# Performance work log

Hardware: AMD Instinct MI355X
Metric: run time of the kernel (lower is better)

## Reference

```python
import jax, jax.numpy as jnp
import numpy as np

X = 512; Y = 512; C = 3; NK = 15
DT = 0.2; DD = 2; SIGMA = 0.95
THETA_X = 2.0; N_EXP = 2.0
K_SIZE = 16

# mesh-grid positions, cell centers at +0.5 (matches construct_mesh_grid)
POS = (jnp.stack(jnp.meshgrid(jnp.arange(X), jnp.arange(Y), indexing='ij'), axis=-1) + 0.5).astype(jnp.float32)  # [X,Y,2]


def _dwconv(img, k):
    # img [X,Y,C'] -> depthwise 3x3 cross-correlation with 'same' zero padding (matches torch conv2d)
    z = img.transpose(2, 0, 1)[None]                      # [1,C',X,Y]
    kern = jnp.tile(k[None, None], (z.shape[1], 1, 1, 1))  # [C',1,3,3]
    out = jax.lax.conv_general_dilated(z, kern, (1, 1), 'SAME', feature_group_count=z.shape[1])
    return out[0].transpose(1, 2, 0)


def _sobel(img):
    # returns [X,Y,2,C'] with (sy, sx) stacked on axis 2, matching torch code order
    kx = jnp.array([[-1., 0., 1.], [-2., 0., 2.], [-1., 0., 1.]], jnp.float32)
    return jnp.stack([_dwconv(img, kx.T), _dwconv(img, kx)], axis=2)


def _reintegrate(grid, F):
    # Flow-Lenia reintegration tracking: 25 static roll offsets, fused accumulation
    ma = DD - SIGMA
    mu = POS[..., None] + jnp.clip(DT * F, -ma, ma)  # [X,Y,2,C]
    mu = jnp.clip(mu, SIGMA, X - SIGMA)
    clip_hi = min(1.0, 2.0 * SIGMA)
    inv_area = 1.0 / (4.0 * SIGMA ** 2)
    acc = jnp.zeros_like(grid)
    for dx in range(-DD, DD + 1):
        for dy in range(-DD, DD + 1):
            gridR = jnp.roll(grid, (dx, dy), (0, 1))
            muR = jnp.roll(mu, (dx, dy), (0, 1))
            sz = 0.5 - jnp.abs(POS[..., None] - muR) + SIGMA
            area = jnp.prod(jnp.clip(sz, 0.0, clip_hi), axis=2) * inv_area  # [X,Y,C]
            acc = acc + gridR * area
    return acc


def _forward(x, Ks, m, s, h, w_c1, c0):
    # spectral kernels: normalize, fftshift, fft2 (matches construct_kernels)
    Ksn = Ks / Ks.sum(axis=(0, 1), keepdims=True)
    fk = jnp.fft.fft2(jnp.fft.fftshift(Ksn, axes=(0, 1)), axes=(0, 1))  # [X,Y,NK] complex
    fXs = jnp.fft.fft2(x, axes=(0, 1))
    Us = jnp.fft.ifft2(fk * fXs[:, :, c0], axes=(0, 1)).real            # [X,Y,NK]
    # growth * h (note: h appears again inside w_c1, faithful to original double multiply)
    Gs = (jnp.exp(-(((Us - m) / s) ** 2) * 0.5) * 2.0 - 1.0) * h
    Hs = jnp.einsum('xyk,kc->xyc', Gs, w_c1)                             # [X,Y,C]
    grad_u = _sobel(Hs)                                                  # [X,Y,2,C]
    grad_x = _sobel(x.sum(-1, keepdims=True))                            # [X,Y,2,1]
    alpha = jnp.clip((x[:, :, None, :] / THETA_X) ** N_EXP, 0.0, 1.0)    # [X,Y,1,C]
    F = grad_u * (1.0 - alpha) - grad_x * alpha                          # [X,Y,2,C]
    return _reintegrate(x, F)


def setup_inputs() -> dict:
    key = jax.random.key(0)
    k1, k2, k3, k4, k5 = jax.random.split(key, 5)
    x = jax.random.uniform(k1, (X, Y, C), jnp.float32)
    # ring kernels per construct_kernels (non-sparse branch)
    mg = np.mgrid[-X // 2:X // 2, -Y // 2:Y // 2]
    base = np.linalg.norm(mg, axis=0).astype(np.float32)
    ks_list = []
    for i in range(NK):
        r = 0.6 + 0.04 * i
        D = base / ((K_SIZE + 15) * r)
        sig = 0.5 * (np.tanh(-(D - 1.0) * 10.0 / 2.0) + 1.0)
        bell = np.exp(-(D - 0.5) ** 2 / 0.15)
        ks_list.append(sig * bell)
    Ks = jnp.asarray(np.stack(ks_list, -1).astype(np.float32))
    m = 0.1 + 0.3 * jax.random.uniform(k2, (NK,), jnp.float32)
    s = 0.03 + 0.15 * jax.random.uniform(k3, (NK,), jnp.float32)
    h = 0.3 + 0.7 * jax.random.uniform(k4, (NK,), jnp.float32)
    c0 = jax.random.randint(k5, (NK,), 0, C, jnp.int32)
    c1 = jnp.arange(NK) % C
    w_c1 = jax.nn.one_hot(c1, C, dtype=jnp.float32) * h[:, None]
    return {"x": x, "Ks": Ks, "m": m, "s": s, "h": h, "w_c1": w_c1, "c0": c0}


def reference(x, Ks, m, s, h, w_c1, c0):
    return _forward(x, Ks, m, s, h, w_c1, c0)
```

## Files before the change

kernel.cpp:

```cpp
#include <hip/hip_runtime.h>
#include <math.h>

#define NPIX 262144
#define NKER 15
#define PI_F 3.14159265358979323846f
#define HW 264
#define CS 578
#define SK(n) ((n) + ((n) >> 3))

__device__ __forceinline__ float2 cadd(float2 a, float2 b) { return make_float2(a.x + b.x, a.y + b.y); }
__device__ __forceinline__ float2 csub(float2 a, float2 b) { return make_float2(a.x - b.x, a.y - b.y); }
__device__ __forceinline__ float2 cmul(float2 a, float2 b) {
  return make_float2(a.x * b.x - a.y * b.y, a.x * b.y + a.y * b.x);
}

__device__ __forceinline__ void fft_roots(int lane, float2* w1, float2* wh) {
  float s, c;
  sincosf(-2.0f * PI_F * (float)lane / 512.0f, &s, &c);
  *w1 = make_float2(c, s);
  int h = lane & ~7;
  *wh = make_float2(__shfl(c, h, 64), __shfl(s, h, 64));
}

template <bool INV>
__device__ __forceinline__ void dft8(float2 a[8]) {
  const float R = 0.70710678118654752f;
  float2 t0 = cadd(a[0], a[4]), u0 = csub(a[0], a[4]);
  float2 t1 = cadd(a[1], a[5]), u1 = csub(a[1], a[5]);
  float2 t2 = cadd(a[2], a[6]), u2 = csub(a[2], a[6]);
  float2 t3 = cadd(a[3], a[7]), u3 = csub(a[3], a[7]);
  u1 = INV ? make_float2(R * (u1.x - u1.y), R * (u1.x + u1.y))
           : make_float2(R * (u1.x + u1.y), R * (u1.y - u1.x));
  u2 = INV ? make_float2(-u2.y, u2.x) : make_float2(u2.y, -u2.x);
  u3 = INV ? make_float2(-R * (u3.x + u3.y), R * (u3.x - u3.y))
           : make_float2(R * (u3.y - u3.x), -R * (u3.x + u3.y));
  float2 e0 = cadd(t0, t2), f0 = csub(t0, t2);
  float2 e1 = cadd(t1, t3), f1 = csub(t1, t3);
  f1 = INV ? make_float2(-f1.y, f1.x) : make_float2(f1.y, -f1.x);
  float2 g0 = cadd(u0, u2), h0 = csub(u0, u2);
  float2 g1 = cadd(u1, u3), h1 = csub(u1, u3);
  h1 = INV ? make_float2(-h1.y, h1.x) : make_float2(h1.y, -h1.x);
  a[0] = cadd(e0, e1); a[4] = csub(e0, e1);
  a[2] = cadd(f0, f1); a[6] = csub(f0, f1);
  a[1] = cadd(g0, g1); a[5] = csub(g0, g1);
  a[3] = cadd(h0, h1); a[7] = csub(h0, h1);
}

template <bool INV>
__device__ __forceinline__ void fft512_r8(float2 a[8], float2* buf, int lane,
                                          float2 w1, float2 wh) {
  float2 wa = INV ? make_float2(w1.x, -w1.y) : w1;
  float2 wb = INV ? make_float2(wh.x, -wh.y) : wh;
  dft8<INV>(a);
  {
    float2 tq = wa;
    a[1] = cmul(a[1], tq);
#pragma unroll
    for (int q = 2; q < 8; ++q) { tq = cmul(tq, wa); a[q] = cmul(a[q], tq); }
  }
#pragma unroll
  for (int q = 0; q < 8; ++q) buf[9 * lane + q] = a[q];
#pragma unroll
  for (int q = 0; q < 8; ++q) a[q] = buf[SK(lane + 64 * q)];
  dft8<INV>(a);
  {
    float2 tq = wb;
    a[1] = cmul(a[1], tq);
#pragma unroll
    for (int q = 2; q < 8; ++q) { tq = cmul(tq, wb); a[q] = cmul(a[q], tq); }
  }
  int h = lane & ~7;
  int b2 = 9 * h + (lane - h);
#pragma unroll
  for (int q = 0; q < 8; ++q) buf[b2 + 9 * q] = a[q];
#pragma unroll
  for (int q = 0; q < 8; ++q) a[q] = buf[SK(lane + 64 * q)];
  dft8<INV>(a);
}

__device__ __forceinline__ void split_store_halfplane(float2 a[8], float2* buf, int lane,
                                                      float2* d0, float2* d1) {
#pragma unroll
  for (int q = 0; q < 8; ++q) buf[SK(lane + 64 * q)] = a[q];
#pragma unroll
  for (int q = 0; q < 4; ++q) {
    int v = lane + 64 * q;
    int mir = (512 - v) & 511;
    float2 P = a[q];
    float2 Qc = buf[SK(mir)];
    float2 Q = make_float2(Qc.x, -Qc.y);
    d0[v] = make_float2(0.5f * (P.x + Q.x), 0.5f * (P.y + Q.y));
    d1[v] = make_float2(0.5f * (P.y - Q.y), -0.5f * (P.x - Q.x));
  }
  if (lane == 0) {
    float2 P = a[4];
    d0[256] = make_float2(P.x, 0.f);
    d1[256] = make_float2(P.y, 0.f);
  }
}

__global__ void rows_all(const float* __restrict__ Ks, const float* __restrict__ x,
                         float* __restrict__ partial, float2* __restrict__ AkH,
                         float2* __restrict__ AxH) {
  __shared__ float krow[512 * NKER];
  __shared__ float2 scr[8][CS];
  __shared__ float psum[480];
  int t = threadIdx.x, wave = t >> 6, lane = t & 63;
  float2 w1, wh;
  fft_roots(lane, &w1, &wh);
  if (blockIdx.x < 512) {
    int b = blockIdx.x;
    int rs = (b + 256) & 511;
    const float2* src = (const float2*)Ks + (size_t)rs * 3840;
    float2* kr2 = (float2*)krow;
    for (int i = t; i < 3840; i += 512) kr2[i] = src[i];
    __syncthreads();
    if (t < 480) {
      int k = t >> 5, yg = t & 31;
      float s = 0.f;
      int base = yg * 16;
#pragma unroll
      for (int y = 0; y < 16; ++y) s += krow[(base + y) * NKER + k];
      psum[t] = s;
    }
    {
      int k1 = 2 * wave, k2 = k1 + 1;
      float2 a[8];
#pragma unroll
      for (int q = 0; q < 8; ++q) {
        int ys = (lane + 64 * q + 256) & 511;
        float re = krow[ys * NKER + k1];
        float im = (k2 < NKER) ? krow[ys * NKER + k2] : 0.f;
        a[q] = make_float2(re, im);
      }
      fft512_r8<false>(a, &scr[wave][0], lane, w1, wh);
      float2* d0 = AkH + ((size_t)k1 * 512 + b) * HW;
      float2* d1 = AkH + ((size_t)k2 * 512 + b) * HW;
      split_store_halfplane(a, &scr[wave][0], lane, d0, d1);
    }
    __syncthreads();
    if (t < NKER) {
      float s = 0.f;
#pragma unroll
      for (int g = 0; g < 32; ++g) s += psum[(t << 5) + g];
      partial[b * 16 + t] = s;
    }
  } else {
    int job = (blockIdx.x - 512) * 8 + wave;
    int c = job >> 8;
    int rp = job & 255;
    int r0 = rp, r1 = rp + 256;
    float2 a[8];
#pragma unroll
    for (int q = 0; q < 8; ++q) {
      int y = lane + 64 * q;
      a[q] = make_float2(x[((size_t)r0 * 512 + y) * 3 + c],
                         x[((size_t)r1 * 512 + y) * 3 + c]);
    }
    fft512_r8<false>(a, &scr[wave][0], lane, w1, wh);
    float2* d0 = AxH + ((size_t)c * 512 + r0) * HW;
    float2* d1 = AxH + ((size_t)c * 512 + r1) * HW;
    split_store_halfplane(a, &scr[wave][0], lane, d0, d1);
  }
}

__global__ void fused_cols(float2* __restrict__ AkH, const float2* __restrict__ AxH,
                           const int* __restrict__ c0, const float* __restrict__ partial,
                           float* __restrict__ sums) {
  __shared__ float2 buf[8 * CS];
  __shared__ float red[512];
  int t = threadIdx.x;
  if (blockIdx.x == 33) {
    if (blockIdx.y != 0) return;
    int k = t & 15, g = t >> 4;
    float acc = 0.f;
    for (int b = g; b < 512; b += 32) acc += partial[b * 16 + k];
    red[t] = acc;
    __syncthreads();
    if (t < 16) {
      float s = 0.f;
#pragma unroll
      for (int g2 = 0; g2 < 32; ++g2) s += red[g2 * 16 + t];
      sums[t] = s;
    }
    return;
  }
  int col0 = blockIdx.x * 8, k = blockIdx.y;
  int c = t >> 6, lane = t & 63;
  float2 w1, wh;
  fft_roots(lane, &w1, &wh);
  const float2* bx = AxH + (size_t)c0[k] * 512 * HW;
  float2* bk = AkH + (size_t)k * 512 * HW;
#pragma unroll
  for (int u = 0; u < 8; ++u) {
    int idx = (u << 9) + t;
    int row = idx >> 3, cc = idx & 7;
    buf[cc * CS + SK(row)] = bx[(size_t)row * HW + col0 + cc];
  }
  __syncthreads();
  float2 xh[8];
#pragma unroll
  for (int q = 0; q < 8; ++q) xh[q] = buf[c * CS + SK(lane + 64 * q)];
  fft512_r8<false>(xh, &buf[c * CS], lane, w1, wh);
  __syncthreads();
#pragma unroll
  for (int u = 0; u < 8; ++u) {
    int idx = (u << 9) + t;
    int row = idx >> 3, cc = idx & 7;
    buf[cc * CS + SK(row)] = bk[(size_t)row * HW + col0 + cc];
  }
  __syncthreads();
  float2 a[8];
#pragma unroll
  for (int q = 0; q < 8; ++q) a[q] = buf[c * CS + SK(lane + 64 * q)];
  fft512_r8<false>(a, &buf[c * CS], lane, w1, wh);
#pragma unroll
  for (int q = 0; q < 8; ++q) a[q] = cmul(a[q], xh[q]);
  fft512_r8<true>(a, &buf[c * CS], lane, w1, wh);
#pragma unroll
  for (int q = 0; q < 8; ++q) buf[c * CS + SK(lane + 64 * q)] = a[q];
  __syncthreads();
#pragma unroll
  for (int u = 0; u < 8; ++u) {
    int idx = (u << 9) + t;
    int row = idx >> 3, cc = idx & 7;
    bk[(size_t)row * HW + col0 + cc] = buf[cc * CS + SK(row)];
  }
}

__global__ void irows_growth_combine(const float2* __restrict__ AkH,
                                     const float* __restrict__ sums,
                                     const float* __restrict__ m, const float* __restrict__ s,
                                     const float* __restrict__ h, const float* __restrict__ w,
                                     float* __restrict__ Hs) {
  __shared__ float2 scr[8][CS];
  __shared__ float accL[4][3][512];
  __shared__ float mk[16], isk[16], hk[16], wk[16][3], sck[16];
  int t = threadIdx.x, wave = t >> 6, lane = t & 63;
  int row = blockIdx.x;
  if (t < NKER) {
    mk[t] = m[t]; isk[t] = 1.0f / s[t]; hk[t] = h[t];
    sck[t] = 1.0f / (sums[t] * 262144.0f);
    wk[t][0] = w[t * 3 + 0]; wk[t][1] = w[t * 3 + 1]; wk[t][2] = w[t * 3 + 2];
  }
  __syncthreads();
  float2 w1, wh;
  fft_roots(lane, &w1, &wh);
  float acc[3][8];
#pragma unroll
  for (int cc = 0; cc < 3; ++cc)
#pragma unroll
    for (int q = 0; q < 8; ++q) acc[cc][q] = 0.f;
  {
    int slot = wave;
    int k1 = 2 * slot, k2 = 2 * slot + 1;
    bool dual = (k2 < NKER);
    const float2* p1 = AkH + ((size_t)k1 * 512 + row) * HW;
    const float2* p2 = AkH + ((size_t)(dual ? k2 : k1) * 512 + row) * HW;
    float2 a[8];
#pragma unroll
    for (int q = 0; q < 8; ++q) {
      int v = lane + 64 * q;
      if (v <= 256) {
        float2 A1 = p1[v];
        float2 A2 = dual ? p2[v] : make_float2(0.f, 0.f);
        a[q] = make_float2(A1.x - A2.y, A1.y + A2.x);
      } else {
        int mi = 512 - v;
        float2 A1 = p1[mi];
        float2 A2 = dual ? p2[mi] : make_float2(0.f, 0.f);
        a[q] = make_float2(A1.x + A2.y, -A1.y + A2.x);
      }
    }
    fft512_r8<true>(a, &scr[wave][0], lane, w1, wh);
    float m1 = mk[k1], i1 = isk[k1], h1 = hk[k1], s1 = sck[k1];
    float w10 = wk[k1][0], w11 = wk[k1][1], w12 = wk[k1][2];
#pragma unroll
    for (int q = 0; q < 8; ++q) {
      float tt = (a[q].x * s1 - m1) * i1;
      float g = (expf(-0.5f * tt * tt) * 2.0f - 1.0f) * h1;
      acc[0][q] += g * w10; acc[1][q] += g * w11; acc[2][q] += g * w12;
    }
    if (dual) {
      float m2 = mk[k2], i2 = isk[k2], h2 = hk[k2], s2 = sck[k2];
      float w20 = wk[k2][0], w21 = wk[k2][1], w22 = wk[k2][2];
#pragma unroll
      for (int q = 0; q < 8; ++q) {
        float tt = (a[q].y * s2 - m2) * i2;
        float g = (expf(-0.5f * tt * tt) * 2.0f - 1.0f) * h2;
        acc[0][q] += g * w20; acc[1][q] += g * w21; acc[2][q] += g * w22;
      }
    }
  }
  if (wave < 4) {
#pragma unroll
    for (int cc = 0; cc < 3; ++cc)
#pragma unroll
      for (int q = 0; q < 8; ++q) accL[wave][cc][lane + 64 * q] = acc[cc][q];
  }
  __syncthreads();
  if (wave >= 4) {
#pragma unroll
    for (int cc = 0; cc < 3; ++cc)
#pragma unroll
      for (int q = 0; q < 8; ++q) accL[wave - 4][cc][lane + 64 * q] += acc[cc][q];
  }
  __syncthreads();
#pragma unroll
  for (int cc = 0; cc < 3; ++cc) {
    float v = accL[0][cc][t] + accL[1][cc][t] + accL[2][cc][t] + accL[3][cc][t];
    Hs[(size_t)cc * NPIX + (size_t)row * 512 + t] = v;
  }
}

__global__ void flow_reint(const float* __restrict__ x, const float* __restrict__ Hs,
                           float* __restrict__ out) {
  __shared__ float muT[20 * 20 * 6];
  __shared__ float xT[20 * 20 * 3];
  int ox = (blockIdx.x >> 5) << 4;
  int oy = (blockIdx.x & 31) << 4;
  for (int i = threadIdx.x; i < 400; i += 256) {
    int hi = i / 20, hj = i % 20;
    int qx = (ox - 2 + hi) & 511, qy = (oy - 2 + hj) & 511;
    float syH0 = 0.f, syH1 = 0.f, syH2 = 0.f;
    float sxH0 = 0.f, sxH1 = 0.f, sxH2 = 0.f;
    float syX = 0.f, sxX = 0.f;
#pragma unroll
    for (int di = -1; di <= 1; ++di) {
#pragma unroll
      for (int dj = -1; dj <= 1; ++dj) {
        if (di == 0 && dj == 0) continue;
        int xi = qx + di, yj = qy + dj;
        if ((unsigned)xi >= 512u || (unsigned)yj >= 512u) continue;
        float wy = (float)di * ((dj == 0) ? 2.f : 1.f);
        float wx = (float)dj * ((di == 0) ? 2.f : 1.f);
        int q = (xi << 9) | yj;
        float h0 = Hs[q], h1 = Hs[NPIX + q], h2 = Hs[2 * NPIX + q];
        syH0 += wy * h0; syH1 += wy * h1; syH2 += wy * h2;
        sxH0 += wx * h0; sxH1 += wx * h1; sxH2 += wx * h2;
        float xs = x[(size_t)q * 3 + 0] + x[(size_t)q * 3 + 1] + x[(size_t)q * 3 + 2];
        syX += wy * xs; sxX += wx * xs;
      }
    }
    int qp = (qx << 9) | qy;
    float cxq = (float)qx + 0.5f, cyq = (float)qy + 0.5f;
    float syH[3] = {syH0, syH1, syH2};
    float sxH[3] = {sxH0, sxH1, sxH2};
    int b6 = i * 6, b3 = i * 3;
#pragma unroll
    for (int c = 0; c < 3; ++c) {
      float xc = x[(size_t)qp * 3 + c];
      xT[b3 + c] = xc;
      float tt = xc * 0.5f;
      float alpha = fminf(tt * tt, 1.0f);
      float F0 = syH[c] * (1.f - alpha) - syX * alpha;
      float F1 = sxH[c] * (1.f - alpha) - sxX * alpha;
      float m0 = cxq + fminf(fmaxf(0.2f * F0, -1.05f), 1.05f);
      float m1 = cyq + fminf(fmaxf(0.2f * F1, -1.05f), 1.05f);
      muT[b6 + c]     = fminf(fmaxf(m0, 0.95f), 511.05f);
      muT[b6 + 3 + c] = fminf(fmaxf(m1, 0.95f), 511.05f);
    }
  }
  __syncthreads();
  int o = threadIdx.x;
  int lx = o >> 4, ly = o & 15;
  int px_ = ox + lx, py_ = oy + ly;
  float cx = (float)px_ + 0.5f, cy = (float)py_ + 0.5f;
  float a0 = 0.f, a1 = 0.f, a2 = 0.f;
#pragma unroll
  for (int dx = -2; dx <= 2; ++dx) {
    int hi = lx + 2 - dx;
#pragma unroll
    for (int dy = -2; dy <= 2; ++dy) {
      int hj = ly + 2 - dy;
      int b6 = (hi * 20 + hj) * 6, b3 = (hi * 20 + hj) * 3;
      float wv;
      wv = fminf(fmaxf(1.45f - fabsf(cx - muT[b6 + 0]), 0.f), 1.f) *
           fminf(fmaxf(1.45f - fabsf(cy - muT[b6 + 3]), 0.f), 1.f);
      a0 += xT[b3 + 0] * wv;
      wv = fminf(fmaxf(1.45f - fabsf(cx - muT[b6 + 1]), 0.f), 1.f) *
           fminf(fmaxf(1.45f - fabsf(cy - muT[b6 + 4]), 0.f), 1.f);
      a1 += xT[b3 + 1] * wv;
      wv = fminf(fmaxf(1.45f - fabsf(cx - muT[b6 + 2]), 0.f), 1.f) *
           fminf(fmaxf(1.45f - fabsf(cy - muT[b6 + 5]), 0.f), 1.f);
      a2 += xT[b3 + 2] * wv;
    }
  }
  const float inv_area = 0.27700831f;
  size_t p = (size_t)((px_ << 9) | py_);
  out[p * 3 + 0] = a0 * inv_area;
  out[p * 3 + 1] = a1 * inv_area;
  out[p * 3 + 2] = a2 * inv_area;
}

extern "C" void kernel_launch(void* const* d_in, const int* in_sizes, int n_in,
                              void* d_out, int out_size, void* d_ws, size_t ws_size,
                              hipStream_t stream) {
  const float* x    = (const float*)d_in[0];
  const float* Ks   = (const float*)d_in[1];
  const float* m    = (const float*)d_in[2];
  const float* s    = (const float*)d_in[3];
  const float* h    = (const float*)d_in[4];
  const float* w_c1 = (const float*)d_in[5];
  const int*   c0   = (const int*)d_in[6];
  float* out = (float*)d_out;

  char* ws = (char*)d_ws;
  size_t off = 0;
  float* sums    = (float*)(ws + off); off += 1024;
  float* partial = (float*)(ws + off); off += 512 * 16 * 4;
  float2* AxH  = (float2*)(ws + off); off += (size_t)3 * 512 * HW * 8;
  float2* AkH  = (float2*)(ws + off); off += (size_t)16 * 512 * HW * 8;
  float*  Hs   = (float*)(ws + off);  off += (size_t)3 * NPIX * 4;

  rows_all<<<608, 512, 0, stream>>>(Ks, x, partial, AkH, AxH);
  fused_cols<<<dim3(34, NKER), 512, 0, stream>>>(AkH, AxH, c0, partial, sums);
  irows_growth_combine<<<512, 512, 0, stream>>>(AkH, sums, m, s, h, w_c1, Hs);
  flow_reint<<<1024, 256, 0, stream>>>(x, Hs, out);
}
```

Before: 133.6 us.

## Precompute twiddle tables, split x column FFT into own kernel, tile flow inputs in LDS

```diff
diff --git a/kernel.cpp b/kernel.cpp
--- a/kernel.cpp
+++ b/kernel.cpp
@@ -13,13 +13,30 @@
 __device__ __forceinline__ float2 cmul(float2 a, float2 b) {
   return make_float2(a.x * b.x - a.y * b.y, a.x * b.y + a.y * b.x);
 }
-
-__device__ __forceinline__ void fft_roots(int lane, float2* w1, float2* wh) {
+__device__ __forceinline__ float2 cmulc(float2 a, float2 b) {
+  return make_float2(a.x * b.x + a.y * b.y, a.y * b.x - a.x * b.y);
+}
+
+__device__ __forceinline__ void build_tw(int lane, float2* pA, float2* pB) {
   float s, c;
   sincosf(-2.0f * PI_F * (float)lane / 512.0f, &s, &c);
-  *w1 = make_float2(c, s);
+  float2 w1 = make_float2(c, s);
   int h = lane & ~7;
-  *wh = make_float2(__shfl(c, h, 64), __shfl(s, h, 64));
+  float2 wh = make_float2(__shfl(c, h, 64), __shfl(s, h, 64));
+  pA[0] = w1;
+  pA[1] = cmul(w1, w1);
+  pA[2] = cmul(pA[1], w1);
+  pA[3] = cmul(pA[1], pA[1]);
+  pA[4] = cmul(pA[3], w1);
+  pA[5] = cmul(pA[3], pA[1]);
+  pA[6] = cmul(pA[3], pA[2]);
+  pB[0] = wh;
+  pB[1] = cmul(wh, wh);
+  pB[2] = cmul(pB[1], wh);
+  pB[3] = cmul(pB[1], pB[1]);
+  pB[4] = cmul(pB[3], wh);
+  pB[5] = cmul(pB[3], pB[1]);
+  pB[6] = cmul(pB[3], pB[2]);
 }
 
 template <bool INV>
@@ -48,27 +65,17 @@
 
 template <bool INV>
 __device__ __forceinline__ void fft512_r8(float2 a[8], float2* buf, int lane,
-                                          float2 w1, float2 wh) {
-  float2 wa = INV ? make_float2(w1.x, -w1.y) : w1;
-  float2 wb = INV ? make_float2(wh.x, -wh.y) : wh;
+                                          const float2* pA, const float2* pB) {
   dft8<INV>(a);
-  {
-    float2 tq = wa;
-    a[1] = cmul(a[1], tq);
-#pragma unroll
-    for (int q = 2; q < 8; ++q) { tq = cmul(tq, wa); a[q] = cmul(a[q], tq); }
-  }
+#pragma unroll
+  for (int q = 1; q < 8; ++q) a[q] = INV ? cmulc(a[q], pA[q - 1]) : cmul(a[q], pA[q - 1]);
 #pragma unroll
   for (int q = 0; q < 8; ++q) buf[9 * lane + q] = a[q];
 #pragma unroll
   for (int q = 0; q < 8; ++q) a[q] = buf[SK(lane + 64 * q)];
   dft8<INV>(a);
-  {
-    float2 tq = wb;
-    a[1] = cmul(a[1], tq);
-#pragma unroll
-    for (int q = 2; q < 8; ++q) { tq = cmul(tq, wb); a[q] = cmul(a[q], tq); }
-  }
+#pragma unroll
+  for (int q = 1; q < 8; ++q) a[q] = INV ? cmulc(a[q], pB[q - 1]) : cmul(a[q], pB[q - 1]);
   int h = lane & ~7;
   int b2 = 9 * h + (lane - h);
 #pragma unroll
@@ -99,15 +106,16 @@
   }
 }
 
-__global__ void rows_all(const float* __restrict__ Ks, const float* __restrict__ x,
-                         float* __restrict__ partial, float2* __restrict__ AkH,
-                         float2* __restrict__ AxH) {
+__global__ __launch_bounds__(512, 4) void rows_all(
+    const float* __restrict__ Ks, const float* __restrict__ x,
+    float* __restrict__ partial, float2* __restrict__ AkH,
+    float2* __restrict__ AxH) {
   __shared__ float krow[512 * NKER];
   __shared__ float2 scr[8][CS];
   __shared__ float psum[480];
   int t = threadIdx.x, wave = t >> 6, lane = t & 63;
-  float2 w1, wh;
-  fft_roots(lane, &w1, &wh);
+  float2 pA[7], pB[7];
+  build_tw(lane, pA, pB);
   if (blockIdx.x < 512) {
     int b = blockIdx.x;
     int rs = (b + 256) & 511;
@@ -133,7 +141,7 @@
         float im = (k2 < NKER) ? krow[ys * NKER + k2] : 0.f;
         a[q] = make_float2(re, im);
       }
-      fft512_r8<false>(a, &scr[wave][0], lane, w1, wh);
+      fft512_r8<false>(a, &scr[wave][0], lane, pA, pB);
       float2* d0 = AkH + ((size_t)k1 * 512 + b) * HW;
       float2* d1 = AkH + ((size_t)k2 * 512 + b) * HW;
       split_store_halfplane(a, &scr[wave][0], lane, d0, d1);
@@ -157,16 +165,41 @@
       a[q] = make_float2(x[((size_t)r0 * 512 + y) * 3 + c],
                          x[((size_t)r1 * 512 + y) * 3 + c]);
     }
-    fft512_r8<false>(a, &scr[wave][0], lane, w1, wh);
+    fft512_r8<false>(a, &scr[wave][0], lane, pA, pB);
     float2* d0 = AxH + ((size_t)c * 512 + r0) * HW;
     float2* d1 = AxH + ((size_t)c * 512 + r1) * HW;
     split_store_halfplane(a, &scr[wave][0], lane, d0, d1);
   }
 }
 
-__global__ void fused_cols(float2* __restrict__ AkH, const float2* __restrict__ AxH,
-                           const int* __restrict__ c0, const float* __restrict__ partial,
-                           float* __restrict__ sums) {
+__global__ __launch_bounds__(512, 4) void xcols(const float2* __restrict__ AxH,
+                                                float2* __restrict__ FxT) {
+  __shared__ float2 buf[8 * CS];
+  int t = threadIdx.x, c = t >> 6, lane = t & 63;
+  int col0 = blockIdx.x << 3, ch = blockIdx.y;
+  float2 pA[7], pB[7];
+  build_tw(lane, pA, pB);
+  const float2* bx = AxH + (size_t)ch * 512 * HW;
+#pragma unroll
+  for (int u = 0; u < 8; ++u) {
+    int idx = (u << 9) + t;
+    int row = idx >> 3, cc = idx & 7;
+    buf[cc * CS + SK(row)] = bx[(size_t)row * HW + col0 + cc];
+  }
+  __syncthreads();
+  float2 a[8];
+#pragma unroll
+  for (int q = 0; q < 8; ++q) a[q] = buf[c * CS + SK(lane + 64 * q)];
+  fft512_r8<false>(a, &buf[c * CS], lane, pA, pB);
+  float2* dst = FxT + ((size_t)ch * HW + col0 + c) * 512;
+#pragma unroll
+  for (int q = 0; q < 8; ++q) dst[lane + 64 * q] = a[q];
+}
+
+__global__ __launch_bounds__(512, 4) void fused_cols(
+    float2* __restrict__ AkH, const float2* __restrict__ FxT,
+    const int* __restrict__ c0, const float* __restrict__ partial,
+    float* __restrict__ sums) {
   __shared__ float2 buf[8 * CS];
   __shared__ float red[512];
   int t = threadIdx.x;
@@ -185,38 +218,29 @@
     }
     return;
   }
-  int col0 = blockIdx.x * 8, k = blockIdx.y;
+  int col0 = blockIdx.x << 3, k = blockIdx.y;
   int c = t >> 6, lane = t & 63;
-  float2 w1, wh;
-  fft_roots(lane, &w1, &wh);
-  const float2* bx = AxH + (size_t)c0[k] * 512 * HW;
+  float2 pA[7], pB[7];
+  build_tw(lane, pA, pB);
   float2* bk = AkH + (size_t)k * 512 * HW;
-#pragma unroll
-  for (int u = 0; u < 8; ++u) {
-    int idx = (u << 9) + t;
-    int row = idx >> 3, cc = idx & 7;
-    buf[cc * CS + SK(row)] = bx[(size_t)row * HW + col0 + cc];
-  }
-  __syncthreads();
-  float2 xh[8];
-#pragma unroll
-  for (int q = 0; q < 8; ++q) xh[q] = buf[c * CS + SK(lane + 64 * q)];
-  fft512_r8<false>(xh, &buf[c * CS], lane, w1, wh);
-  __syncthreads();
 #pragma unroll
   for (int u = 0; u < 8; ++u) {
     int idx = (u << 9) + t;
     int row = idx >> 3, cc = idx & 7;
     buf[cc * CS + SK(row)] = bk[(size_t)row * HW + col0 + cc];
   }
+  const float2* fx = FxT + ((size_t)c0[k] * HW + col0 + c) * 512;
+  float2 xq[8];
+#pragma unroll
+  for (int q = 0; q < 8; ++q) xq[q] = fx[lane + 64 * q];
   __syncthreads();
   float2 a[8];
 #pragma unroll
   for (int q = 0; q < 8; ++q) a[q] = buf[c * CS + SK(lane + 64 * q)];
-  fft512_r8<false>(a, &buf[c * CS], lane, w1, wh);
-#pragma unroll
-  for (int q = 0; q < 8; ++q) a[q] = cmul(a[q], xh[q]);
-  fft512_r8<true>(a, &buf[c * CS], lane, w1, wh);
+  fft512_r8<false>(a, &buf[c * CS], lane, pA, pB);
+#pragma unroll
+  for (int q = 0; q < 8; ++q) a[q] = cmul(a[q], xq[q]);
+  fft512_r8<true>(a, &buf[c * CS], lane, pA, pB);
 #pragma unroll
   for (int q = 0; q < 8; ++q) buf[c * CS + SK(lane + 64 * q)] = a[q];
   __syncthreads();
@@ -228,11 +252,11 @@
   }
 }
 
-__global__ void irows_growth_combine(const float2* __restrict__ AkH,
-                                     const float* __restrict__ sums,
-                                     const float* __restrict__ m, const float* __restrict__ s,
-                                     const float* __restrict__ h, const float* __restrict__ w,
-                                     float* __restrict__ Hs) {
+__global__ __launch_bounds__(512, 4) void irows_growth_combine(
+    const float2* __restrict__ AkH, const float* __restrict__ sums,
+    const float* __restrict__ m, const float* __restrict__ s,
+    const float* __restrict__ h, const float* __restrict__ w,
+    float* __restrict__ Hs) {
   __shared__ float2 scr[8][CS];
   __shared__ float accL[4][3][512];
   __shared__ float mk[16], isk[16], hk[16], wk[16][3], sck[16];
@@ -244,8 +268,8 @@
     wk[t][0] = w[t * 3 + 0]; wk[t][1] = w[t * 3 + 1]; wk[t][2] = w[t * 3 + 2];
   }
   __syncthreads();
-  float2 w1, wh;
-  fft_roots(lane, &w1, &wh);
+  float2 pA[7], pB[7];
+  build_tw(lane, pA, pB);
   float acc[3][8];
 #pragma unroll
   for (int cc = 0; cc < 3; ++cc)
@@ -272,7 +296,7 @@
         a[q] = make_float2(A1.x + A2.y, -A1.y + A2.x);
       }
     }
-    fft512_r8<true>(a, &scr[wave][0], lane, w1, wh);
+    fft512_r8<true>(a, &scr[wave][0], lane, pA, pB);
     float m1 = mk[k1], i1 = isk[k1], h1 = hk[k1], s1 = sck[k1];
     float w10 = wk[k1][0], w11 = wk[k1][1], w12 = wk[k1][2];
 #pragma unroll
@@ -315,10 +339,21 @@
 
 __global__ void flow_reint(const float* __restrict__ x, const float* __restrict__ Hs,
                            float* __restrict__ out) {
-  __shared__ float muT[20 * 20 * 6];
-  __shared__ float xT[20 * 20 * 3];
+  __shared__ float tS[7][496];
+  __shared__ float muT[400 * 6];
   int ox = (blockIdx.x >> 5) << 4;
   int oy = (blockIdx.x & 31) << 4;
+  for (int i = threadIdx.x; i < 484; i += 256) {
+    int li = i / 22, lj = i % 22;
+    int qx = (ox - 3 + li) & 511, qy = (oy - 3 + lj) & 511;
+    int q = (qx << 9) | qy;
+    float h0 = Hs[q], h1 = Hs[NPIX + q], h2 = Hs[2 * NPIX + q];
+    float x0 = x[(size_t)q * 3 + 0], x1 = x[(size_t)q * 3 + 1], x2 = x[(size_t)q * 3 + 2];
+    tS[0][i] = h0; tS[1][i] = h1; tS[2][i] = h2;
+    tS[3][i] = x0 + x1 + x2;
+    tS[4][i] = x0; tS[5][i] = x1; tS[6][i] = x2;
+  }
+  __syncthreads();
   for (int i = threadIdx.x; i < 400; i += 256) {
     int hi = i / 20, hj = i % 20;
     int qx = (ox - 2 + hi) & 511, qy = (oy - 2 + hj) & 511;
@@ -332,25 +367,24 @@
         if (di == 0 && dj == 0) continue;
         int xi = qx + di, yj = qy + dj;
         if ((unsigned)xi >= 512u || (unsigned)yj >= 512u) continue;
+        int l = (hi + 1 + di) * 22 + (hj + 1 + dj);
         float wy = (float)di * ((dj == 0) ? 2.f : 1.f);
         float wx = (float)dj * ((di == 0) ? 2.f : 1.f);
-        int q = (xi << 9) | yj;
-        float h0 = Hs[q], h1 = Hs[NPIX + q], h2 = Hs[2 * NPIX + q];
+        float h0 = tS[0][l], h1 = tS[1][l], h2 = tS[2][l];
         syH0 += wy * h0; syH1 += wy * h1; syH2 += wy * h2;
         sxH0 += wx * h0; sxH1 += wx * h1; sxH2 += wx * h2;
-        float xs = x[(size_t)q * 3 + 0] + x[(size_t)q * 3 + 1] + x[(size_t)q * 3 + 2];
+        float xs = tS[3][l];
         syX += wy * xs; sxX += wx * xs;
       }
     }
-    int qp = (qx << 9) | qy;
+    int lc = (hi + 1) * 22 + (hj + 1);
     float cxq = (float)qx + 0.5f, cyq = (float)qy + 0.5f;
     float syH[3] = {syH0, syH1, syH2};
     float sxH[3] = {sxH0, sxH1, sxH2};
-    int b6 = i * 6, b3 = i * 3;
+    int b6 = i * 6;
 #pragma unroll
     for (int c = 0; c < 3; ++c) {
-      float xc = x[(size_t)qp * 3 + c];
-      xT[b3 + c] = xc;
+      float xc = tS[4 + c][lc];
       float tt = xc * 0.5f;
       float alpha = fminf(tt * tt, 1.0f);
       float F0 = syH[c] * (1.f - alpha) - syX * alpha;
@@ -373,17 +407,18 @@
 #pragma unroll
     for (int dy = -2; dy <= 2; ++dy) {
       int hj = ly + 2 - dy;
-      int b6 = (hi * 20 + hj) * 6, b3 = (hi * 20 + hj) * 3;
+      int b6 = (hi * 20 + hj) * 6;
+      int lb = (hi + 1) * 22 + (hj + 1);
       float wv;
       wv = fminf(fmaxf(1.45f - fabsf(cx - muT[b6 + 0]), 0.f), 1.f) *
            fminf(fmaxf(1.45f - fabsf(cy - muT[b6 + 3]), 0.f), 1.f);
-      a0 += xT[b3 + 0] * wv;
+      a0 += tS[4][lb] * wv;
       wv = fminf(fmaxf(1.45f - fabsf(cx - muT[b6 + 1]), 0.f), 1.f) *
            fminf(fmaxf(1.45f - fabsf(cy - muT[b6 + 4]), 0.f), 1.f);
-      a1 += xT[b3 + 1] * wv;
+      a1 += tS[5][lb] * wv;
       wv = fminf(fmaxf(1.45f - fabsf(cx - muT[b6 + 2]), 0.f), 1.f) *
            fminf(fmaxf(1.45f - fabsf(cy - muT[b6 + 5]), 0.f), 1.f);
-      a2 += xT[b3 + 2] * wv;
+      a2 += tS[6][lb] * wv;
     }
   }
   const float inv_area = 0.27700831f;
@@ -411,10 +446,12 @@
   float* partial = (float*)(ws + off); off += 512 * 16 * 4;
   float2* AxH  = (float2*)(ws + off); off += (size_t)3 * 512 * HW * 8;
   float2* AkH  = (float2*)(ws + off); off += (size_t)16 * 512 * HW * 8;
+  float2* FxT  = (float2*)(ws + off); off += (size_t)3 * HW * 512 * 8;
   float*  Hs   = (float*)(ws + off);  off += (size_t)3 * NPIX * 4;
 
   rows_all<<<608, 512, 0, stream>>>(Ks, x, partial, AkH, AxH);
-  fused_cols<<<dim3(34, NKER), 512, 0, stream>>>(AkH, AxH, c0, partial, sums);
+  xcols<<<dim3(33, 3), 512, 0, stream>>>(AxH, FxT);
+  fused_cols<<<dim3(34, NKER), 512, 0, stream>>>(AkH, FxT, c0, partial, sums);
   irows_growth_combine<<<512, 512, 0, stream>>>(AkH, sums, m, s, h, w_c1, Hs);
   flow_reint<<<1024, 256, 0, stream>>>(x, Hs, out);
 }
```

Result: faster. 128.1 us (-4.1%).
